# Performance work log

Measured on AMD Instinct MI355X. Metric: run time of the kernel, lower is better.

## Reference

```python
import jax, jax.numpy as jnp
import numpy as np

N_NODES = 4096
N_SUBS = 1024
NUM_FEATURES = 128
HIDDEN = 512
NHEADS = 8
DHEAD = HIDDEN // NHEADS
NUM_LAYERS = 2
EDGE_PROB = 0.01
NEG_INF = -1e9


def _make_adj(key, n, p):
    a = (jax.random.uniform(key, (n, n)) < p).astype(jnp.float32)
    return jnp.maximum(a, jnp.eye(n, dtype=jnp.float32))  # self-loops


def setup_inputs() -> dict:
    key = jax.random.key(0)
    ks = jax.random.split(key, 12)
    x = jax.random.normal(ks[0], (N_NODES, NUM_FEATURES), dtype=jnp.float32)
    adj_node = _make_adj(ks[1], N_NODES, EDGE_PROB)
    adj_substation = _make_adj(ks[2], N_SUBS, 4 * EDGE_PROB)
    seg_ids = jnp.sort(jax.random.randint(ks[3], (N_NODES,), 0, N_SUBS, dtype=jnp.int32))
    s = 0.05
    lin_w = jax.random.normal(ks[4], (NUM_FEATURES, HIDDEN), dtype=jnp.float32) * s
    lin_b = jnp.zeros((HIDDEN,), dtype=jnp.float32)
    node_W = jax.random.normal(ks[5], (NUM_LAYERS, HIDDEN, HIDDEN), dtype=jnp.float32) * s
    node_asrc = jax.random.normal(ks[6], (NUM_LAYERS, NHEADS, DHEAD), dtype=jnp.float32) * s
    node_adst = jax.random.normal(ks[7], (NUM_LAYERS, NHEADS, DHEAD), dtype=jnp.float32) * s
    sub_W = jax.random.normal(ks[8], (NUM_LAYERS, HIDDEN, HIDDEN), dtype=jnp.float32) * s
    sub_asrc = jax.random.normal(ks[9], (NUM_LAYERS, NHEADS, DHEAD), dtype=jnp.float32) * s
    sub_adst = jax.random.normal(ks[10], (NUM_LAYERS, NHEADS, DHEAD), dtype=jnp.float32) * s
    return {"x": x, "adj_node": adj_node, "adj_substation": adj_substation,
            "seg_ids": seg_ids, "lin_w": lin_w, "lin_b": lin_b,
            "node_W": node_W, "node_asrc": node_asrc, "node_adst": node_adst,
            "sub_W": sub_W, "sub_asrc": sub_asrc, "sub_adst": sub_adst}


def _gat_layer(h, adj, W, a_src, a_dst):
    # h: [N, F]; adj: [N, N]; W: [F, F]; a_src/a_dst: [H, Dh]
    n = h.shape[0]
    Wh = (h @ W).reshape(n, NHEADS, DHEAD)               # [N, H, Dh]
    f_src = jnp.einsum('nhd,hd->hn', Wh, a_src)          # [H, N]
    f_dst = jnp.einsum('nhd,hd->hn', Wh, a_dst)          # [H, N]
    e = jax.nn.leaky_relu(f_src[:, :, None] + f_dst[:, None, :], 0.2)  # [H, N, N]
    e = jnp.where(adj[None] > 0, e, NEG_INF)
    alpha = jax.nn.softmax(e, axis=-1)                   # [H, N, N]
    out = jnp.einsum('hij,jhd->ihd', alpha, Wh).reshape(n, NHEADS * DHEAD)
    return jax.nn.elu(out)


def _stacked_gats(h, adj, Ws, asrcs, adsts):
    # Faithful to the source bug: x is never rebound, each layer sees the
    # original input; the last layer's output is returned.
    out = h
    for i in range(Ws.shape[0]):
        out = _gat_layer(h, adj, Ws[i], asrcs[i], adsts[i])
    return out


def _pool_mean(h, seg_ids, num_segments):
    sums = jax.ops.segment_sum(h, seg_ids, num_segments=num_segments)
    counts = jax.ops.segment_sum(jnp.ones((h.shape[0], 1), h.dtype), seg_ids,
                                 num_segments=num_segments)
    return sums / jnp.maximum(counts, 1.0)


def reference(x, adj_node, adj_substation, seg_ids, lin_w, lin_b,
              node_W, node_asrc, node_adst, sub_W, sub_asrc, sub_adst):
    h = x @ lin_w + lin_b                                  # [N, HIDDEN]
    h = _stacked_gats(h, adj_node, node_W, node_asrc, node_adst)
    s = _pool_mean(h, seg_ids, N_SUBS)                     # [S, HIDDEN]
    s = _stacked_gats(s, adj_substation, sub_W, sub_asrc, sub_adst)
    return s
```

## Files before the change

### kernel.cpp

```cpp
#include <hip/hip_runtime.h>
#include <hip/hip_bf16.h>
#include <hip/hip_fp16.h>
#include <math.h>

#define N_NODES 4096
#define N_SUBS  1024
#define NFEAT   128
#define HIDDEN  512
#define NHEADS  8
#define DHEAD   64
#define CAP     128
#define ROWG    4
#define CAPP    (CAP + 4)

typedef float vfloat4 __attribute__((ext_vector_type(4)));

struct alignas(16) h8 { __half2 a, b, c, d; };

#define NB_EXTRACT (N_NODES / 4 + N_SUBS / 4)
#define NB_GEMM    (8 * 3 * 16)
#define BM 64
#define BN 64
#define BK 16

__global__ __launch_bounds__(256) void phase1(const float* __restrict__ adj_n,
                                              const float* __restrict__ adj_s,
                                              int* __restrict__ cnt_n,
                                              int* __restrict__ nbr_n,
                                              int* __restrict__ cnt_s,
                                              int* __restrict__ nbr_s,
                                              const float* __restrict__ lin_w,
                                              const float* __restrict__ node_W1,
                                              const float* __restrict__ lin_b,
                                              float* __restrict__ Wpart,
                                              float* __restrict__ bpart) {
    const int tid = threadIdx.x;
    if (blockIdx.x < NB_EXTRACT) {
        const int w = tid >> 6;
        const int lane = tid & 63;
        const float* adj;
        int N, row;
        int* cnt;
        int* nbr;
        if (blockIdx.x < N_NODES / 4) {
            adj = adj_n; N = N_NODES; cnt = cnt_n; nbr = nbr_n;
            row = blockIdx.x * 4 + w;
        } else {
            adj = adj_s; N = N_SUBS; cnt = cnt_s; nbr = nbr_s;
            row = (blockIdx.x - N_NODES / 4) * 4 + w;
        }
        const vfloat4* rowp = (const vfloat4*)(adj + (size_t)row * N);
        int* nrow = nbr + (row << 7);
        const int n4 = N >> 2;
        int c = 0;
        const unsigned long long below = (1ull << lane) - 1ull;
        for (int c4 = lane; c4 < n4; c4 += 64) {
            const vfloat4 v = __builtin_nontemporal_load(&rowp[c4]);
            const int col = c4 << 2;
            unsigned long long m;
            bool p;
            p = v.x > 0.0f; m = __ballot(p);
            if (p) { int q = c + __popcll(m & below); if (q < CAP) nrow[q] = col; }
            c += __popcll(m);
            p = v.y > 0.0f; m = __ballot(p);
            if (p) { int q = c + __popcll(m & below); if (q < CAP) nrow[q] = col + 1; }
            c += __popcll(m);
            p = v.z > 0.0f; m = __ballot(p);
            if (p) { int q = c + __popcll(m & below); if (q < CAP) nrow[q] = col + 2; }
            c += __popcll(m);
            p = v.w > 0.0f; m = __ballot(p);
            if (p) { int q = c + __popcll(m & below); if (q < CAP) nrow[q] = col + 3; }
            c += __popcll(m);
        }
        if (lane == 0) cnt[row] = c < CAP ? c : CAP;
        return;
    }
    {
        const int b = blockIdx.x - NB_EXTRACT;
        const int bn = (b & 7) * BN;
        const int rem = b >> 3;
        const int by = rem % 3;
        const int bz = rem / 3;
        const int M = NFEAT, N = HIDDEN, K = HIDDEN;
        const int k_chunk = K / 16;
        const int k_start = bz * k_chunk;
        __shared__ float As[BK][BM + 4];
        __shared__ float Bs[BK][BN + 4];
        if (by == 2) {
            const int q = tid >> 6;
            const int n = tid & 63;
            const int sub = k_chunk >> 2;
            const int kb = k_start + q * sub;
            float s = 0.0f;
            for (int k = 0; k < sub; k++)
                s += lin_b[kb + k] * node_W1[(size_t)(kb + k) * N + bn + n];
            float* red = (float*)As;
            red[q * 64 + n] = s;
            __syncthreads();
            if (q == 0)
                bpart[bz * N + bn + n] = red[n] + red[64 + n] + red[128 + n] + red[192 + n];
            return;
        }
        const int bm = by * BM;
        float* Cw = Wpart + (size_t)bz * M * N;
        const int tr = tid >> 4;
        const int tc = tid & 15;
        const int am = tid >> 2;
        const int ak4 = (tid & 3) * 4;
        const int bk = tid >> 4;
        const int bn0 = (tid & 15) * 4;
        float acc[4][4] = {};
        for (int k0 = k_start; k0 < k_start + k_chunk; k0 += BK) {
            const float4 va = *(const float4*)&lin_w[(size_t)(bm + am) * K + k0 + ak4];
            const float4 vb = *(const float4*)&node_W1[(size_t)(k0 + bk) * N + bn + bn0];
            As[ak4 + 0][am] = va.x;
            As[ak4 + 1][am] = va.y;
            As[ak4 + 2][am] = va.z;
            As[ak4 + 3][am] = va.w;
            *(float4*)&Bs[bk][bn0] = vb;
            __syncthreads();
#pragma unroll
            for (int k = 0; k < BK; k++) {
                const float4 a4 = *(const float4*)&As[k][tr * 4];
                const float4 b4 = *(const float4*)&Bs[k][tc * 4];
                const float a[4] = {a4.x, a4.y, a4.z, a4.w};
                const float bb[4] = {b4.x, b4.y, b4.z, b4.w};
#pragma unroll
                for (int i = 0; i < 4; i++)
#pragma unroll
                    for (int j = 0; j < 4; j++)
                        acc[i][j] += a[i] * bb[j];
            }
            __syncthreads();
        }
#pragma unroll
        for (int i = 0; i < 4; i++) {
            const int m = bm + tr * 4 + i;
            float4 o = {acc[i][0], acc[i][1], acc[i][2], acc[i][3]};
            *(float4*)&Cw[(size_t)m * N + bn + tc * 4] = o;
        }
    }
}

__global__ __launch_bounds__(256) void gemm_f32(const float* __restrict__ A,
                                                const float* __restrict__ B,
                                                const float* __restrict__ bias,
                                                float* __restrict__ C,
                                                int M, int N, int K, int k_chunk,
                                                const float* __restrict__ asrc,
                                                const float* __restrict__ adst,
                                                float* __restrict__ fs,
                                                float* __restrict__ fd,
                                                __half* __restrict__ C_h) {
    __shared__ float As[BK][BM + 4];
    __shared__ float Bs[BK][BN + 4];
    const int tid = threadIdx.x;
    const int bm = blockIdx.y * BM;
    const int bn = blockIdx.x * BN;
    const int k_start = blockIdx.z * k_chunk;
    const int k_end = (k_start + k_chunk) < K ? (k_start + k_chunk) : K;
    float* Cw = C + (size_t)blockIdx.z * M * N;
    const int tr = tid >> 4;
    const int tc = tid & 15;
    const int am = tid >> 2;
    const int ak4 = (tid & 3) * 4;
    const int bk = tid >> 4;
    const int bn0 = (tid & 15) * 4;
    float acc[4][4] = {};
    for (int k0 = k_start; k0 < k_end; k0 += BK) {
        const float4 va = *(const float4*)&A[(size_t)(bm + am) * K + k0 + ak4];
        const float4 vb = *(const float4*)&B[(size_t)(k0 + bk) * N + bn + bn0];
        As[ak4 + 0][am] = va.x;
        As[ak4 + 1][am] = va.y;
        As[ak4 + 2][am] = va.z;
        As[ak4 + 3][am] = va.w;
        *(float4*)&Bs[bk][bn0] = vb;
        __syncthreads();
#pragma unroll
        for (int k = 0; k < BK; k++) {
            const float4 a4 = *(const float4*)&As[k][tr * 4];
            const float4 b4 = *(const float4*)&Bs[k][tc * 4];
            const float a[4] = {a4.x, a4.y, a4.z, a4.w};
            const float b[4] = {b4.x, b4.y, b4.z, b4.w};
#pragma unroll
            for (int i = 0; i < 4; i++)
#pragma unroll
                for (int j = 0; j < 4; j++)
                    acc[i][j] += a[i] * b[j];
        }
        __syncthreads();
    }
#pragma unroll
    for (int i = 0; i < 4; i++) {
        const int m = bm + tr * 4 + i;
        if (bias) {
            const float4 bv = *(const float4*)&bias[bn + tc * 4];
            acc[i][0] += bv.x; acc[i][1] += bv.y; acc[i][2] += bv.z; acc[i][3] += bv.w;
        }
        if (C_h) {
            __half2 p0 = __floats2half2_rn(acc[i][0], acc[i][1]);
            __half2 p1 = __floats2half2_rn(acc[i][2], acc[i][3]);
            __half2* hp = (__half2*)&C_h[(size_t)m * N + bn + tc * 4];
            hp[0] = p0;
            hp[1] = p1;
        } else {
            float4 o = {acc[i][0], acc[i][1], acc[i][2], acc[i][3]};
            *(float4*)&Cw[(size_t)m * N + bn + tc * 4] = o;
        }
    }
    if (asrc) {
        const int h = blockIdx.x;
        const float4 as4 = *(const float4*)&asrc[h * DHEAD + tc * 4];
        const float4 ad4 = *(const float4*)&adst[h * DHEAD + tc * 4];
#pragma unroll
        for (int i = 0; i < 4; i++) {
            float vs = acc[i][0] * as4.x + acc[i][1] * as4.y +
                       acc[i][2] * as4.z + acc[i][3] * as4.w;
            float vd = acc[i][0] * ad4.x + acc[i][1] * ad4.y +
                       acc[i][2] * ad4.z + acc[i][3] * ad4.w;
#pragma unroll
            for (int off = 1; off < 16; off <<= 1) {
                vs += __shfl_xor(vs, off, 64);
                vd += __shfl_xor(vd, off, 64);
            }
            if (tc == 0) {
                const int m = bm + tr * 4 + i;
                fs[h * M + m] = vs;
                fd[h * M + m] = vd;
            }
        }
    }
}

__global__ __launch_bounds__(256) void reduce_both(const float* __restrict__ p1,
                                                   float* __restrict__ o1,
                                                   int len1, int nz1,
                                                   const float* __restrict__ p2,
                                                   float* __restrict__ o2,
                                                   int len2, int nz2,
                                                   int blocks1) {
    if ((int)blockIdx.x < blocks1) {
        const int i = blockIdx.x * 256 + threadIdx.x;
        if (i < len1) {
            float s = 0.0f;
            for (int z = 0; z < nz1; z++) s += p1[(size_t)z * len1 + i];
            o1[i] = s;
        }
    } else {
        const int i = (blockIdx.x - blocks1) * 256 + threadIdx.x;
        if (i < len2) {
            float s = 0.0f;
            for (int z = 0; z < nz2; z++) s += p2[(size_t)z * len2 + i];
            o2[i] = s;
        }
    }
}

__global__ __launch_bounds__(512) void reduce_fsfd(const float* __restrict__ part,
                                                   float* __restrict__ wh,
                                                   const float* __restrict__ asrc,
                                                   const float* __restrict__ adst,
                                                   float* __restrict__ fs,
                                                   float* __restrict__ fd,
                                                   int M, int nz) {
    const int n = blockIdx.x;
    const int tid = threadIdx.x;
    float v = 0.0f;
    for (int z = 0; z < nz; z++)
        v += part[((size_t)z * M + n) * HIDDEN + tid];
    wh[(size_t)n * HIDDEN + tid] = v;
    const int h = tid >> 6;
    const int d = tid & 63;
    float vs = v * asrc[h * DHEAD + d];
    float vd = v * adst[h * DHEAD + d];
#pragma unroll
    for (int off = 32; off >= 1; off >>= 1) {
        vs += __shfl_xor(vs, off, 64);
        vd += __shfl_xor(vd, off, 64);
    }
    if (d == 0) {
        fs[h * M + n] = vs;
        fd[h * M + n] = vd;
    }
}

__device__ __forceinline__ void gat_softmax(const float* __restrict__ fs,
                                            const float* __restrict__ fd,
                                            const int* snbr, float (*ex)[CAP + 1],
                                            int C, int i, int N, int tid) {
    const int h = tid >> 6;
    const int lane = tid & 63;
    const float fsi = fs[h * N + i];
    const float* __restrict__ fdh = fd + h * N;
    float m = -1e30f;
    for (int k = lane; k < C; k += 64) {
        float e = fsi + fdh[snbr[k]];
        e = e > 0.0f ? e : 0.2f * e;
        ex[h][k] = e;
        m = fmaxf(m, e);
    }
#pragma unroll
    for (int off = 32; off >= 1; off >>= 1) m = fmaxf(m, __shfl_xor(m, off, 64));
    float ssum = 0.0f;
    for (int k = lane; k < C; k += 64) {
        float v = __expf(ex[h][k] - m);
        ex[h][k] = v;
        ssum += v;
    }
#pragma unroll
    for (int off = 32; off >= 1; off >>= 1) ssum += __shfl_xor(ssum, off, 64);
    const float inv = 1.0f / ssum;
    for (int k = lane; k < C; k += 64) ex[h][k] *= inv;
}

__global__ __launch_bounds__(512) void gat_agg_h(const __half* __restrict__ Wh,
                                                 const float* __restrict__ fs,
                                                 const float* __restrict__ fd,
                                                 const int* __restrict__ cnt,
                                                 const int* __restrict__ nbr,
                                                 float* __restrict__ out, int N) {
    __shared__ int snbr[8][CAP];
    __shared__ float al[8][NHEADS][CAPP];
    const int w = threadIdx.x >> 6;
    const int lane = threadIdx.x & 63;
    const int i = blockIdx.x * 8 + w;
    int C = cnt[i];
    C = C < CAP ? C : CAP;
    for (int k = lane; k < C; k += 64) snbr[w][k] = nbr[(i << 7) + k];
    const int h = lane >> 3;
    const int s = lane & 7;
    const float fsi = fs[h * N + i];
    const float* __restrict__ fdh = fd + h * N;
    float m = -1e30f;
    for (int k = s; k < C; k += 8) {
        float e = fsi + fdh[snbr[w][k]];
        e = e > 0.0f ? e : 0.2f * e;
        al[w][h][k] = e;
        m = fmaxf(m, e);
    }
    m = fmaxf(m, __shfl_xor(m, 1, 64));
    m = fmaxf(m, __shfl_xor(m, 2, 64));
    m = fmaxf(m, __shfl_xor(m, 4, 64));
    float ssum = 0.0f;
    for (int k = s; k < C; k += 8) {
        float v = __expf(al[w][h][k] - m);
        al[w][h][k] = v;
        ssum += v;
    }
    ssum += __shfl_xor(ssum, 1, 64);
    ssum += __shfl_xor(ssum, 2, 64);
    ssum += __shfl_xor(ssum, 4, 64);
    const float inv = 1.0f / ssum;
    for (int k = s; k < C; k += 8) al[w][h][k] *= inv;
    float acc[8] = {};
    int k = 0;
    for (; k + 8 <= C; k += 8) {
        h8 ww[8];
        float aa[8];
#pragma unroll
        for (int u = 0; u < 8; u++) {
            ww[u] = *(const h8*)&Wh[(size_t)snbr[w][k + u] * HIDDEN + 8 * lane];
            aa[u] = al[w][h][k + u];
        }
#pragma unroll
        for (int u = 0; u < 8; u++) {
            float2 f;
            f = __half22float2(ww[u].a); acc[0] += aa[u] * f.x; acc[1] += aa[u] * f.y;
            f = __half22float2(ww[u].b); acc[2] += aa[u] * f.x; acc[3] += aa[u] * f.y;
            f = __half22float2(ww[u].c); acc[4] += aa[u] * f.x; acc[5] += aa[u] * f.y;
            f = __half22float2(ww[u].d); acc[6] += aa[u] * f.x; acc[7] += aa[u] * f.y;
        }
    }
    for (; k < C; k++) {
        const h8 w0 = *(const h8*)&Wh[(size_t)snbr[w][k] * HIDDEN + 8 * lane];
        const float a0 = al[w][h][k];
        float2 f;
        f = __half22float2(w0.a); acc[0] += a0 * f.x; acc[1] += a0 * f.y;
        f = __half22float2(w0.b); acc[2] += a0 * f.x; acc[3] += a0 * f.y;
        f = __half22float2(w0.c); acc[4] += a0 * f.x; acc[5] += a0 * f.y;
        f = __half22float2(w0.d); acc[6] += a0 * f.x; acc[7] += a0 * f.y;
    }
#pragma unroll
    for (int e = 0; e < 8; e++)
        acc[e] = acc[e] > 0.0f ? acc[e] : __expf(acc[e]) - 1.0f;
    float4 o0 = {acc[0], acc[1], acc[2], acc[3]};
    float4 o1 = {acc[4], acc[5], acc[6], acc[7]};
    float4* op = (float4*)&out[(size_t)i * HIDDEN + 8 * lane];
    op[0] = o0;
    op[1] = o1;
}

__global__ __launch_bounds__(512) void gat_agg_f(const float* __restrict__ Wh,
                                                 const float* __restrict__ fs,
                                                 const float* __restrict__ fd,
                                                 const int* __restrict__ cnt,
                                                 const int* __restrict__ nbr,
                                                 float* __restrict__ out, int N) {
    __shared__ int snbr[CAP];
    __shared__ float ex[NHEADS][CAP + 1];
    __shared__ float sacc[ROWG][HIDDEN];
    const int i = blockIdx.x;
    const int tid = threadIdx.x;
    int C = cnt[i];
    C = C < CAP ? C : CAP;
    for (int k = tid; k < C; k += 512) snbr[k] = nbr[(i << 7) + k];
    __syncthreads();
    gat_softmax(fs, fd, snbr, ex, C, i, N, tid);
    __syncthreads();
    const int g = tid >> 7;
    const int t = tid & 127;
    const int hh = t >> 4;
    float4 acc = {0.f, 0.f, 0.f, 0.f};
    int k = g;
    for (; k + 3 * ROWG < C; k += 4 * ROWG) {
        const int j0 = snbr[k];
        const int j1 = snbr[k + ROWG];
        const int j2 = snbr[k + 2 * ROWG];
        const int j3 = snbr[k + 3 * ROWG];
        const float a0 = ex[hh][k];
        const float a1 = ex[hh][k + ROWG];
        const float a2 = ex[hh][k + 2 * ROWG];
        const float a3 = ex[hh][k + 3 * ROWG];
        const float4 w0 = *(const float4*)&Wh[(size_t)j0 * HIDDEN + 4 * t];
        const float4 w1 = *(const float4*)&Wh[(size_t)j1 * HIDDEN + 4 * t];
        const float4 w2 = *(const float4*)&Wh[(size_t)j2 * HIDDEN + 4 * t];
        const float4 w3 = *(const float4*)&Wh[(size_t)j3 * HIDDEN + 4 * t];
        acc.x += a0 * w0.x + a1 * w1.x + a2 * w2.x + a3 * w3.x;
        acc.y += a0 * w0.y + a1 * w1.y + a2 * w2.y + a3 * w3.y;
        acc.z += a0 * w0.z + a1 * w1.z + a2 * w2.z + a3 * w3.z;
        acc.w += a0 * w0.w + a1 * w1.w + a2 * w2.w + a3 * w3.w;
    }
    for (; k < C; k += ROWG) {
        const int j0 = snbr[k];
        const float a0 = ex[hh][k];
        const float4 w0 = *(const float4*)&Wh[(size_t)j0 * HIDDEN + 4 * t];
        acc.x += a0 * w0.x; acc.y += a0 * w0.y;
        acc.z += a0 * w0.z; acc.w += a0 * w0.w;
    }
    *(float4*)&sacc[g][4 * t] = acc;
    __syncthreads();
    if (g == 0) {
        float4 r = acc;
#pragma unroll
        for (int gg = 1; gg < ROWG; gg++) {
            const float4 o = *(const float4*)&sacc[gg][4 * t];
            r.x += o.x; r.y += o.y; r.z += o.z; r.w += o.w;
        }
        r.x = r.x > 0.0f ? r.x : __expf(r.x) - 1.0f;
        r.y = r.y > 0.0f ? r.y : __expf(r.y) - 1.0f;
        r.z = r.z > 0.0f ? r.z : __expf(r.z) - 1.0f;
        r.w = r.w > 0.0f ? r.w : __expf(r.w) - 1.0f;
        *(float4*)&out[(size_t)i * HIDDEN + 4 * t] = r;
    }
}

__global__ __launch_bounds__(512) void pool_kernel(const float* __restrict__ hin,
                                                   const int* __restrict__ seg,
                                                   float* __restrict__ sout) {
    const int s = blockIdx.x;
    const int d = threadIdx.x;
    int lo = 0, hi = N_NODES;
    while (lo < hi) { int mid = (lo + hi) >> 1; if (seg[mid] < s) lo = mid + 1; else hi = mid; }
    const int start = lo;
    hi = N_NODES;
    while (lo < hi) { int mid = (lo + hi) >> 1; if (seg[mid] < s + 1) lo = mid + 1; else hi = mid; }
    const int end = lo;
    float acc = 0.0f;
    for (int r = start; r < end; r++) acc += hin[(size_t)r * HIDDEN + d];
    const int c = end - start;
    sout[(size_t)s * HIDDEN + d] = acc / (c > 0 ? (float)c : 1.0f);
}

extern "C" void kernel_launch(void* const* d_in, const int* in_sizes, int n_in,
                              void* d_out, int out_size, void* d_ws, size_t ws_size,
                              hipStream_t stream) {
    const float* x        = (const float*)d_in[0];
    const float* adj_node = (const float*)d_in[1];
    const float* adj_sub  = (const float*)d_in[2];
    const int*   seg_ids  = (const int*)d_in[3];
    const float* lin_w    = (const float*)d_in[4];
    const float* lin_b    = (const float*)d_in[5];
    const float* node_W1    = (const float*)d_in[6]  + HIDDEN * HIDDEN;
    const float* node_asrc1 = (const float*)d_in[7]  + NHEADS * DHEAD;
    const float* node_adst1 = (const float*)d_in[8]  + NHEADS * DHEAD;
    const float* sub_W1     = (const float*)d_in[9]  + HIDDEN * HIDDEN;
    const float* sub_asrc1  = (const float*)d_in[10] + NHEADS * DHEAD;
    const float* sub_adst1  = (const float*)d_in[11] + NHEADS * DHEAD;
    float* out = (float*)d_out;

    char* ws = (char*)d_ws;
    float* bufA  = (float*)(ws);
    float* bufB  = (float*)(ws + (size_t)8 * 1024 * 1024);
    float* fs_n  = (float*)(ws + (size_t)16 * 1024 * 1024);
    float* fd_n  = fs_n + NHEADS * N_NODES;
    float* fs_s  = fd_n + NHEADS * N_NODES;
    float* fd_s  = fs_s + NHEADS * N_SUBS;
    int*   cnt_n = (int*)(fd_s + NHEADS * N_SUBS);
    int*   cnt_s = cnt_n + N_NODES;
    int*   nbr_n = cnt_s + N_SUBS;
    int*   nbr_s = nbr_n + N_NODES * CAP;

    float*  Wpart = bufB;
    float*  Wfuse = bufB + 16 * NFEAT * HIDDEN;
    float*  bpart = Wfuse + NFEAT * HIDDEN;
    float*  bias2 = bpart + 16 * HIDDEN;
    float*  gatom = bufB;
    float*  Spart = bufB;
    __half* wh_n  = (__half*)bufA;
    float*  sp    = bufA;
    float*  wh_s  = bufA + (size_t)N_SUBS * HIDDEN;

    phase1<<<NB_EXTRACT + NB_GEMM, 256, 0, stream>>>(
        adj_node, adj_sub, cnt_n, nbr_n, cnt_s, nbr_s,
        lin_w, node_W1, lin_b, Wpart, bpart);
    reduce_both<<<NFEAT * HIDDEN / 256 + 2, 256, 0, stream>>>(
        Wpart, Wfuse, NFEAT * HIDDEN, 16, bpart, bias2, HIDDEN, 16,
        NFEAT * HIDDEN / 256);
    gemm_f32<<<dim3(HIDDEN / BN, N_NODES / BM, 1), 256, 0, stream>>>(
        x, Wfuse, bias2, nullptr, N_NODES, HIDDEN, NFEAT, NFEAT,
        node_asrc1, node_adst1, fs_n, fd_n, wh_n);
    gat_agg_h<<<N_NODES / 8, 512, 0, stream>>>(wh_n, fs_n, fd_n, cnt_n, nbr_n,
                                               gatom, N_NODES);
    pool_kernel<<<N_SUBS, 512, 0, stream>>>(gatom, seg_ids, sp);
    gemm_f32<<<dim3(HIDDEN / BN, N_SUBS / BM, 4), 256, 0, stream>>>(
        sp, sub_W1, nullptr, Spart, N_SUBS, HIDDEN, HIDDEN, HIDDEN / 4,
        nullptr, nullptr, nullptr, nullptr, nullptr);
    reduce_fsfd<<<N_SUBS, 512, 0, stream>>>(Spart, wh_s, sub_asrc1, sub_adst1,
                                            fs_s, fd_s, N_SUBS, 4);
    gat_agg_f<<<N_SUBS, 512, 0, stream>>>(wh_s, fs_s, fd_s, cnt_s, nbr_s,
                                          out, N_SUBS);
}
```

Before: 201.1 us.

## Restructure substation GAT aggregation to one wavefront per row without block syncs

The fp32 substation aggregation kernel previously used a 512-thread block per row, with a block-wide softmax, four row-groups and a shared-memory reduction. It now mirrors the half-precision node kernel: each 64-lane wavefront owns one row, eight lanes per head compute the softmax with shuffles, and each lane accumulates 8 output columns over all neighbours with 4-way unrolled loads. This removes the __syncthreads barriers and the cross-group reduction. In exchange each row has less parallelism, and the dependent neighbour loop is longer per lane, so latency hiding relies on the unrolled loads.

```diff
diff --git a/kernel.cpp b/kernel.cpp
--- a/kernel.cpp
+++ b/kernel.cpp
@@ -10,7 +10,6 @@
 #define NHEADS  8
 #define DHEAD   64
 #define CAP     128
-#define ROWG    4
 #define CAPP    (CAP + 4)
 
 typedef float vfloat4 __attribute__((ext_vector_type(4)));
@@ -284,35 +283,6 @@
     }
 }
 
-__device__ __forceinline__ void gat_softmax(const float* __restrict__ fs,
-                                            const float* __restrict__ fd,
-                                            const int* snbr, float (*ex)[CAP + 1],
-                                            int C, int i, int N, int tid) {
-    const int h = tid >> 6;
-    const int lane = tid & 63;
-    const float fsi = fs[h * N + i];
-    const float* __restrict__ fdh = fd + h * N;
-    float m = -1e30f;
-    for (int k = lane; k < C; k += 64) {
-        float e = fsi + fdh[snbr[k]];
-        e = e > 0.0f ? e : 0.2f * e;
-        ex[h][k] = e;
-        m = fmaxf(m, e);
-    }
-#pragma unroll
-    for (int off = 32; off >= 1; off >>= 1) m = fmaxf(m, __shfl_xor(m, off, 64));
-    float ssum = 0.0f;
-    for (int k = lane; k < C; k += 64) {
-        float v = __expf(ex[h][k] - m);
-        ex[h][k] = v;
-        ssum += v;
-    }
-#pragma unroll
-    for (int off = 32; off >= 1; off >>= 1) ssum += __shfl_xor(ssum, off, 64);
-    const float inv = 1.0f / ssum;
-    for (int k = lane; k < C; k += 64) ex[h][k] *= inv;
-}
-
 __global__ __launch_bounds__(512) void gat_agg_h(const __half* __restrict__ Wh,
                                                  const float* __restrict__ fs,
                                                  const float* __restrict__ fd,
@@ -390,68 +360,83 @@
     op[1] = o1;
 }
 
-__global__ __launch_bounds__(512) void gat_agg_f(const float* __restrict__ Wh,
+__global__ __launch_bounds__(256) void gat_agg_f(const float* __restrict__ Wh,
                                                  const float* __restrict__ fs,
                                                  const float* __restrict__ fd,
                                                  const int* __restrict__ cnt,
                                                  const int* __restrict__ nbr,
                                                  float* __restrict__ out, int N) {
-    __shared__ int snbr[CAP];
-    __shared__ float ex[NHEADS][CAP + 1];
-    __shared__ float sacc[ROWG][HIDDEN];
-    const int i = blockIdx.x;
-    const int tid = threadIdx.x;
+    __shared__ int snbr[4][CAP];
+    __shared__ float al[4][NHEADS][CAPP];
+    const int w = threadIdx.x >> 6;
+    const int lane = threadIdx.x & 63;
+    const int i = blockIdx.x * 4 + w;
     int C = cnt[i];
     C = C < CAP ? C : CAP;
-    for (int k = tid; k < C; k += 512) snbr[k] = nbr[(i << 7) + k];
-    __syncthreads();
-    gat_softmax(fs, fd, snbr, ex, C, i, N, tid);
-    __syncthreads();
-    const int g = tid >> 7;
-    const int t = tid & 127;
-    const int hh = t >> 4;
-    float4 acc = {0.f, 0.f, 0.f, 0.f};
-    int k = g;
-    for (; k + 3 * ROWG < C; k += 4 * ROWG) {
-        const int j0 = snbr[k];
-        const int j1 = snbr[k + ROWG];
-        const int j2 = snbr[k + 2 * ROWG];
-        const int j3 = snbr[k + 3 * ROWG];
-        const float a0 = ex[hh][k];
-        const float a1 = ex[hh][k + ROWG];
-        const float a2 = ex[hh][k + 2 * ROWG];
-        const float a3 = ex[hh][k + 3 * ROWG];
-        const float4 w0 = *(const float4*)&Wh[(size_t)j0 * HIDDEN + 4 * t];
-        const float4 w1 = *(const float4*)&Wh[(size_t)j1 * HIDDEN + 4 * t];
-        const float4 w2 = *(const float4*)&Wh[(size_t)j2 * HIDDEN + 4 * t];
-        const float4 w3 = *(const float4*)&Wh[(size_t)j3 * HIDDEN + 4 * t];
-        acc.x += a0 * w0.x + a1 * w1.x + a2 * w2.x + a3 * w3.x;
-        acc.y += a0 * w0.y + a1 * w1.y + a2 * w2.y + a3 * w3.y;
-        acc.z += a0 * w0.z + a1 * w1.z + a2 * w2.z + a3 * w3.z;
-        acc.w += a0 * w0.w + a1 * w1.w + a2 * w2.w + a3 * w3.w;
-    }
-    for (; k < C; k += ROWG) {
-        const int j0 = snbr[k];
-        const float a0 = ex[hh][k];
-        const float4 w0 = *(const float4*)&Wh[(size_t)j0 * HIDDEN + 4 * t];
-        acc.x += a0 * w0.x; acc.y += a0 * w0.y;
-        acc.z += a0 * w0.z; acc.w += a0 * w0.w;
-    }
-    *(float4*)&sacc[g][4 * t] = acc;
-    __syncthreads();
-    if (g == 0) {
-        float4 r = acc;
-#pragma unroll
-        for (int gg = 1; gg < ROWG; gg++) {
-            const float4 o = *(const float4*)&sacc[gg][4 * t];
-            r.x += o.x; r.y += o.y; r.z += o.z; r.w += o.w;
-        }
-        r.x = r.x > 0.0f ? r.x : __expf(r.x) - 1.0f;
-        r.y = r.y > 0.0f ? r.y : __expf(r.y) - 1.0f;
-        r.z = r.z > 0.0f ? r.z : __expf(r.z) - 1.0f;
-        r.w = r.w > 0.0f ? r.w : __expf(r.w) - 1.0f;
-        *(float4*)&out[(size_t)i * HIDDEN + 4 * t] = r;
-    }
+    for (int k = lane; k < C; k += 64) snbr[w][k] = nbr[(i << 7) + k];
+    const int h = lane >> 3;
+    const int s = lane & 7;
+    const float fsi = fs[h * N + i];
+    const float* __restrict__ fdh = fd + h * N;
+    float m = -1e30f;
+    for (int k = s; k < C; k += 8) {
+        float e = fsi + fdh[snbr[w][k]];
+        e = e > 0.0f ? e : 0.2f * e;
+        al[w][h][k] = e;
+        m = fmaxf(m, e);
+    }
+    m = fmaxf(m, __shfl_xor(m, 1, 64));
+    m = fmaxf(m, __shfl_xor(m, 2, 64));
+    m = fmaxf(m, __shfl_xor(m, 4, 64));
+    float ssum = 0.0f;
+    for (int k = s; k < C; k += 8) {
+        float v = __expf(al[w][h][k] - m);
+        al[w][h][k] = v;
+        ssum += v;
+    }
+    ssum += __shfl_xor(ssum, 1, 64);
+    ssum += __shfl_xor(ssum, 2, 64);
+    ssum += __shfl_xor(ssum, 4, 64);
+    const float inv = 1.0f / ssum;
+    for (int k = s; k < C; k += 8) al[w][h][k] *= inv;
+    float acc[8] = {};
+    int k = 0;
+    for (; k + 4 <= C; k += 4) {
+        float4 wa[4], wb[4];
+        float aa[4];
+#pragma unroll
+        for (int u = 0; u < 4; u++) {
+            const float4* p = (const float4*)&Wh[(size_t)snbr[w][k + u] * HIDDEN + 8 * lane];
+            wa[u] = p[0];
+            wb[u] = p[1];
+            aa[u] = al[w][h][k + u];
+        }
+#pragma unroll
+        for (int u = 0; u < 4; u++) {
+            acc[0] += aa[u] * wa[u].x; acc[1] += aa[u] * wa[u].y;
+            acc[2] += aa[u] * wa[u].z; acc[3] += aa[u] * wa[u].w;
+            acc[4] += aa[u] * wb[u].x; acc[5] += aa[u] * wb[u].y;
+            acc[6] += aa[u] * wb[u].z; acc[7] += aa[u] * wb[u].w;
+        }
+    }
+    for (; k < C; k++) {
+        const float4* p = (const float4*)&Wh[(size_t)snbr[w][k] * HIDDEN + 8 * lane];
+        const float4 wa = p[0];
+        const float4 wb = p[1];
+        const float a0 = al[w][h][k];
+        acc[0] += a0 * wa.x; acc[1] += a0 * wa.y;
+        acc[2] += a0 * wa.z; acc[3] += a0 * wa.w;
+        acc[4] += a0 * wb.x; acc[5] += a0 * wb.y;
+        acc[6] += a0 * wb.z; acc[7] += a0 * wb.w;
+    }
+#pragma unroll
+    for (int e = 0; e < 8; e++)
+        acc[e] = acc[e] > 0.0f ? acc[e] : __expf(acc[e]) - 1.0f;
+    float4 o0 = {acc[0], acc[1], acc[2], acc[3]};
+    float4 o1 = {acc[4], acc[5], acc[6], acc[7]};
+    float4* op = (float4*)&out[(size_t)i * HIDDEN + 8 * lane];
+    op[0] = o0;
+    op[1] = o1;
 }
 
 __global__ __launch_bounds__(512) void pool_kernel(const float* __restrict__ hin,
@@ -527,6 +512,6 @@
         nullptr, nullptr, nullptr, nullptr, nullptr);
     reduce_fsfd<<<N_SUBS, 512, 0, stream>>>(Spart, wh_s, sub_asrc1, sub_adst1,
                                             fs_s, fd_s, N_SUBS, 4);
-    gat_agg_f<<<N_SUBS, 512, 0, stream>>>(wh_s, fs_s, fd_s, cnt_s, nbr_s,
-                                          out, N_SUBS);
-}
+    gat_agg_f<<<N_SUBS / 4, 256, 0, stream>>>(wh_s, fs_s, fd_s, cnt_s, nbr_s,
+                                              out, N_SUBS);
+}
```

Result: no change. 201.3 us (+0.1%).
